# Optimization experiments

Measured on AMD Instinct MI355X. Metric: run time of the kernel, lower is better.

The kernel has to match this reference:

```python
import jax, jax.numpy as jnp
import numpy as np

B, S, D, H = 4, 4096, 1024, 64

def setup_inputs() -> dict:
    key = jax.random.key(0)
    k1, k2, k3, k4 = jax.random.split(key, 4)
    inp = {
        'input': jax.random.normal(k1, (B, S, D), dtype=jnp.float32),
        'Wq': jax.random.normal(k2, (D, H), dtype=jnp.float32) * (D ** -0.5),
        'Wk': jax.random.normal(k3, (D, H), dtype=jnp.float32) * (D ** -0.5),
        'Wv': jax.random.normal(k4, (D, H), dtype=jnp.float32) * (D ** -0.5),
    }
    return inp

def reference(input, Wq, Wk, Wv):
    # Projections: [B,S,D] @ [D,H] -> [B,S,H]
    q = input @ Wq
    k = input @ Wk
    v = input @ Wv
    head_size = Wq.shape[-1]
    # Scaled scores: [B,S,S]
    scores = jnp.einsum('bqh,bkh->bqk', q, k) * (head_size ** -0.5)
    seq_len = input.shape[1]
    causal = jnp.tril(jnp.ones((seq_len, seq_len), dtype=bool))
    masked = jnp.where(causal, scores, -jnp.inf)
    weights = jax.nn.softmax(masked, axis=-1)
    # dropout p=0.0 -> identity
    return jnp.einsum('bqk,bkh->bqh', weights, v)
```

## Files before the change

### kernel.cpp

```cpp
#include <hip/hip_runtime.h>

#define NS 8

typedef __attribute__((ext_vector_type(8))) short sh8;
typedef __attribute__((ext_vector_type(4))) short sh4;
typedef __attribute__((ext_vector_type(4))) float f4;

#define QSCALE 0.18033688011112042f

typedef const __attribute__((address_space(1))) unsigned int* gas_t;
typedef __attribute__((address_space(3))) unsigned int* las_t;
#define GLD16(g, l) __builtin_amdgcn_global_load_lds((gas_t)(g), (las_t)(l), 16, 0, 0)

static __device__ __forceinline__ unsigned short f2bf(float f) {
  unsigned u = __builtin_bit_cast(unsigned, f);
  u += 0x7fffu + ((u >> 16) & 1u);
  return (unsigned short)(u >> 16);
}
static __device__ __forceinline__ float bf2f(unsigned short s) {
  unsigned u = ((unsigned)s) << 16;
  return __builtin_bit_cast(float, u);
}

__global__ __launch_bounds__(256) void wt_kernel(const float* __restrict__ Wq,
                                                 const float* __restrict__ Wk,
                                                 const float* __restrict__ Wv,
                                                 unsigned short* __restrict__ Wt2) {
  int blk = blockIdx.x;
  int band = blk >> 3;
  int widx = band >> 2;
  const float* W = widx == 0 ? Wq : (widx == 1 ? Wk : Wv);
  int ncol = (band & 3) * 16;
  int t = threadIdx.x;
  int kt = (blk & 7) * 4 + (t >> 6);
  int lane = t & 63, q = lane >> 4, l15 = lane & 15;
  const float* src = W + (size_t)(kt * 32 + q * 8) * 64 + ncol + l15;
  sh8 o;
#pragma unroll
  for (int j = 0; j < 8; ++j) o[j] = (short)f2bf(src[(size_t)j * 64]);
  *(sh8*)&Wt2[((size_t)(band * 32 + kt) * 64 + lane) * 8] = o;
}

__global__ __launch_bounds__(256, 1) void proj_kernel(const float* __restrict__ in,
                                                      const unsigned short* __restrict__ Wt2,
                                                      unsigned short* __restrict__ Qg,
                                                      unsigned short* __restrict__ Kg,
                                                      unsigned short* __restrict__ Vtg) {
  __shared__ __align__(16) char lds[131072];
  int t = threadIdx.x;
  int w = t >> 6, lane = t & 63, q = lane >> 4, l15 = lane & 15;
  int m0 = blockIdx.x * 32;

  const float* ga = in + (size_t)(m0 + (w >> 1) * 16 + l15) * 1024 + q * 8 + (w & 1) * 4;
  const unsigned short* gb = Wt2 + (size_t)(w * 3) * 16384 + lane * 8;

  f4 acc[2][3];
  f4 z = {0.f, 0.f, 0.f, 0.f};
#pragma unroll
  for (int mt = 0; mt < 2; ++mt)
#pragma unroll
    for (int nt = 0; nt < 3; ++nt) acc[mt][nt] = z;

#define STAGE(s, buf)                                                         \
  {                                                                           \
    char* base = lds + (buf) * 65536;                                         \
    const float* gas = ga + (s) * 128;                                        \
    _Pragma("unroll")                                                         \
    for (int kk = 0; kk < 4; ++kk) {                                          \
      GLD16(gas + kk * 32, base + kk * 4096 + w * 1024);                      \
      _Pragma("unroll")                                                       \
      for (int nt = 0; nt < 3; ++nt)                                          \
        GLD16(gb + nt * 16384 + ((s) * 4 + kk) * 512,                         \
              base + 16384 + (kk * 12 + w * 3 + nt) * 1024);                  \
    }                                                                         \
  }

  STAGE(0, 0);
  for (int s = 0; s < 8; ++s) {
    int cur = s & 1;
    __syncthreads();
    if (s + 1 < 8) STAGE(s + 1, cur ^ 1);

    const f4* Af = (const f4*)(lds + cur * 65536);
    const sh8* Bf = (const sh8*)(lds + cur * 65536 + 16384);
#pragma unroll
    for (int kk = 0; kk < 4; ++kk) {
      sh8 bfr[3];
#pragma unroll
      for (int nt = 0; nt < 3; ++nt)
        bfr[nt] = Bf[(kk * 12 + w * 3 + nt) * 64 + lane];
#pragma unroll
      for (int mt = 0; mt < 2; ++mt) {
        f4 lo = Af[kk * 256 + mt * 128 + lane];
        f4 hi = Af[kk * 256 + mt * 128 + 64 + lane];
        sh8 a;
#pragma unroll
        for (int j = 0; j < 4; ++j) {
          a[j] = (short)f2bf(lo[j]);
          a[4 + j] = (short)f2bf(hi[j]);
        }
#pragma unroll
        for (int nt = 0; nt < 3; ++nt)
          acc[mt][nt] = __builtin_amdgcn_mfma_f32_16x16x32_bf16(a, bfr[nt], acc[mt][nt], 0, 0, 0);
      }
    }
  }
#undef STAGE

  float* vred = (float*)lds;
#pragma unroll
  for (int nt = 0; nt < 3; ++nt) {
    int band = w * 3 + nt;
#pragma unroll
    for (int mt = 0; mt < 2; ++mt)
#pragma unroll
      for (int r = 0; r < 4; ++r) {
        int row = mt * 16 + q * 4 + r;
        float v = acc[mt][nt][r];
        if (band < 4) {
          Qg[(size_t)(m0 + row) * 64 + band * 16 + l15] = f2bf(v * QSCALE);
        } else if (band < 8) {
          Kg[(size_t)(m0 + row) * 64 + (band - 4) * 16 + l15] = f2bf(v);
        } else {
          vred[row * 69 + (band - 8) * 16 + l15] = v;
        }
      }
  }
  __syncthreads();
  {
    int h = t >> 2, sl = (t & 3) * 8;
    int bb = m0 >> 12, s0 = m0 & 4095;
    sh8 vv;
#pragma unroll
    for (int j = 0; j < 8; ++j) vv[j] = (short)f2bf(vred[(sl + j) * 69 + h]);
    *(sh8*)&Vtg[(((size_t)(bb * 64 + h)) << 12) + s0 + sl] = vv;
  }
}

__global__ __launch_bounds__(256, 4) void attn_split(const unsigned short* __restrict__ Qg,
                                                     const unsigned short* __restrict__ Kg,
                                                     const unsigned short* __restrict__ Vtg,
                                                     unsigned short* __restrict__ Opart,
                                                     float* __restrict__ Lpart) {
  __shared__ unsigned short Ks[64 * 72];
  __shared__ unsigned short Vs[64 * 72];
  __shared__ unsigned short Pw[4 * 16 * 72];
  int t = threadIdx.x;
  int b = blockIdx.y;
  int qt = 63 - (int)(blockIdx.x >> 3);
  int sp = blockIdx.x & 7;
  int wave = t >> 6, lane = t & 63, quad = lane >> 4, l15 = lane & 15;
  unsigned short* Pws = Pw + wave * 16 * 72;

  int qrow0 = qt * 64 + wave * 16;
  size_t pbase = ((size_t)sp * 4 + b) * 4096;

  int nkt = qt + 1;
  int chunk = (nkt + NS - 1) / NS;
  int t0 = sp * chunk, t1 = min(nkt, t0 + chunk);
  if (t0 >= t1) {
#pragma unroll
    for (int r = 0; r < 4; ++r) {
      size_t row = pbase + qrow0 + quad * 4 + r;
#pragma unroll
      for (int ht = 0; ht < 4; ++ht) Opart[row * 64 + ht * 16 + l15] = 0;
      if (l15 == 0) Lpart[row] = 0.f;
    }
    return;
  }

  sh8 qa[2];
#pragma unroll
  for (int ks = 0; ks < 2; ++ks)
    qa[ks] = *(const sh8*)&Qg[(size_t)((b << 12) + qrow0 + l15) * 64 + ks * 32 + quad * 8];

  sh8 ones;
#pragma unroll
  for (int j = 0; j < 8; ++j) ones[j] = (short)0x3F80;

  f4 o[5];
  f4 z = {0.f, 0.f, 0.f, 0.f};
#pragma unroll
  for (int ht = 0; ht < 5; ++ht) o[ht] = z;

  int r0 = t >> 3, o0 = (t & 7) * 8;
  int r1 = (t + 256) >> 3, o1 = ((t + 256) & 7) * 8;
  const unsigned short* kg0 = Kg + (size_t)((b << 12) + r0) * 64 + o0;
  const unsigned short* kg1 = Kg + (size_t)((b << 12) + r1) * 64 + o1;
  const unsigned short* vg0 = Vtg + (((size_t)(b * 64 + r0)) << 12) + o0;
  const unsigned short* vg1 = Vtg + (((size_t)(b * 64 + r1)) << 12) + o1;

  sh8 kr0, kr1, vr0, vr1;
  {
    size_t ko = (size_t)t0 * 64 * 64;
    kr0 = *(const sh8*)(kg0 + ko); kr1 = *(const sh8*)(kg1 + ko);
    vr0 = *(const sh8*)(vg0 + t0 * 64); vr1 = *(const sh8*)(vg1 + t0 * 64);
  }

  for (int kt = t0; kt < t1; ++kt) {
    __syncthreads();
    *(sh8*)&Ks[r0 * 72 + o0] = kr0;
    *(sh8*)&Ks[r1 * 72 + o1] = kr1;
    *(sh8*)&Vs[r0 * 72 + o0] = vr0;
    *(sh8*)&Vs[r1 * 72 + o1] = vr1;
    if (kt + 1 < t1) {
      size_t ko = (size_t)(kt + 1) * 64 * 64;
      kr0 = *(const sh8*)(kg0 + ko); kr1 = *(const sh8*)(kg1 + ko);
      vr0 = *(const sh8*)(vg0 + (kt + 1) * 64); vr1 = *(const sh8*)(vg1 + (kt + 1) * 64);
    }
    __syncthreads();

    f4 st[4];
#pragma unroll
    for (int nt = 0; nt < 4; ++nt) st[nt] = z;
#pragma unroll
    for (int ks = 0; ks < 2; ++ks) {
#pragma unroll
      for (int nt = 0; nt < 4; ++nt) {
        sh8 kb = *(const sh8*)&Ks[(nt * 16 + l15) * 72 + ks * 32 + quad * 8];
        st[nt] = __builtin_amdgcn_mfma_f32_16x16x32_bf16(kb, qa[ks], st[nt], 0, 0, 0);
      }
    }

    if (kt == nkt - 1) {
      int qrow = qrow0 + l15;
#pragma unroll
      for (int nt = 0; nt < 4; ++nt) {
        int key0 = kt * 64 + nt * 16 + quad * 4;
#pragma unroll
        for (int r = 0; r < 4; ++r)
          if (key0 + r > qrow) st[nt][r] = -__builtin_inff();
      }
    }

#pragma unroll
    for (int nt = 0; nt < 4; ++nt) {
      sh4 pk;
#pragma unroll
      for (int r = 0; r < 4; ++r) pk[r] = (short)f2bf(exp2f(st[nt][r]));
      *(sh4*)&Pws[l15 * 72 + nt * 16 + quad * 4] = pk;
    }
    asm volatile("s_waitcnt lgkmcnt(0)" ::: "memory");

#pragma unroll
    for (int ks = 0; ks < 2; ++ks) {
      sh8 pa = *(const sh8*)&Pws[l15 * 72 + ks * 32 + quad * 8];
#pragma unroll
      for (int ht = 0; ht < 4; ++ht) {
        sh8 vb = *(const sh8*)&Vs[(ht * 16 + l15) * 72 + ks * 32 + quad * 8];
        o[ht] = __builtin_amdgcn_mfma_f32_16x16x32_bf16(pa, vb, o[ht], 0, 0, 0);
      }
      o[4] = __builtin_amdgcn_mfma_f32_16x16x32_bf16(pa, ones, o[4], 0, 0, 0);
    }
  }

#pragma unroll
  for (int r = 0; r < 4; ++r) {
    size_t row = pbase + qrow0 + quad * 4 + r;
#pragma unroll
    for (int ht = 0; ht < 4; ++ht)
      Opart[row * 64 + ht * 16 + l15] = f2bf(o[ht][r]);
    if (l15 == 0) Lpart[row] = o[4][r];
  }
}

__global__ __launch_bounds__(256) void attn_combine(const unsigned short* __restrict__ Opart,
                                                    const float* __restrict__ Lpart,
                                                    float* __restrict__ out) {
  int t = threadIdx.x;
  int r = blockIdx.x * 32 + (t >> 3);
  int h0 = (t & 7) * 8;
  float L = 0.f;
  float acc[8];
#pragma unroll
  for (int j = 0; j < 8; ++j) acc[j] = 0.f;
#pragma unroll
  for (int s = 0; s < NS; ++s) {
    L += Lpart[(size_t)s * 16384 + r];
    sh8 v = *(const sh8*)&Opart[((size_t)s * 16384 + r) * 64 + h0];
#pragma unroll
    for (int j = 0; j < 8; ++j) acc[j] += bf2f((unsigned short)v[j]);
  }
  float inv = 1.f / L;
  f4 o0, o1;
#pragma unroll
  for (int j = 0; j < 4; ++j) { o0[j] = acc[j] * inv; o1[j] = acc[4 + j] * inv; }
  *(f4*)&out[(size_t)r * 64 + h0] = o0;
  *(f4*)&out[(size_t)r * 64 + h0 + 4] = o1;
}

extern "C" void kernel_launch(void* const* d_in, const int* in_sizes, int n_in,
                              void* d_out, int out_size, void* d_ws, size_t ws_size,
                              hipStream_t stream) {
  const float* in = (const float*)d_in[0];
  const float* Wq = (const float*)d_in[1];
  const float* Wk = (const float*)d_in[2];
  const float* Wv = (const float*)d_in[3];
  float* out = (float*)d_out;

  char* ws = (char*)d_ws;
  unsigned short* Wt2   = (unsigned short*)ws;
  unsigned short* Qg    = (unsigned short*)(ws + 393216);
  unsigned short* Kg    = (unsigned short*)(ws + 2490368);
  unsigned short* Vtg   = (unsigned short*)(ws + 4587520);
  unsigned short* Opart = (unsigned short*)(ws + 6684672);
  float*          Lpart = (float*)(ws + 23461888);

  hipLaunchKernelGGL(wt_kernel, dim3(96), dim3(256), 0, stream, Wq, Wk, Wv, Wt2);
  hipLaunchKernelGGL(proj_kernel, dim3(512), dim3(256), 0, stream, in, Wt2, Qg, Kg, Vtg);
  hipLaunchKernelGGL(attn_split, dim3(64 * NS, 4), dim3(256), 0, stream,
                     Qg, Kg, Vtg, Opart, Lpart);
  hipLaunchKernelGGL(attn_combine, dim3(512), dim3(256), 0, stream,
                     Opart, Lpart, out);
}
```

Measured before the change: 150.1 us.

## Widen attention key tile to 128 keys per iteration with larger LDS buffers

Each loop iteration of the split attention kernel now processes 128 keys instead of 64: K and transposed V tiles in LDS are doubled and each thread prefetches four vectors of K and V per step. The P@V phase runs in two 64-key halves reusing the same per-wave P scratch. This halves the number of barrier-separated iterations and loads per key block, at the cost of more LDS and registers (launch bound lowered from 4 to 3 blocks per CU). It also does more masked wasted work on the diagonal tile and makes split chunks coarser, which may hurt load balance.

```diff
diff --git a/kernel.cpp b/kernel.cpp
--- a/kernel.cpp
+++ b/kernel.cpp
@@ -137,13 +137,13 @@
   }
 }
 
-__global__ __launch_bounds__(256, 4) void attn_split(const unsigned short* __restrict__ Qg,
+__global__ __launch_bounds__(256, 3) void attn_split(const unsigned short* __restrict__ Qg,
                                                      const unsigned short* __restrict__ Kg,
                                                      const unsigned short* __restrict__ Vtg,
                                                      unsigned short* __restrict__ Opart,
                                                      float* __restrict__ Lpart) {
-  __shared__ unsigned short Ks[64 * 72];
-  __shared__ unsigned short Vs[64 * 72];
+  __shared__ unsigned short Ks[128 * 72];
+  __shared__ unsigned short Vs[64 * 136];
   __shared__ unsigned short Pw[4 * 16 * 72];
   int t = threadIdx.x;
   int b = blockIdx.y;
@@ -155,9 +155,9 @@
   int qrow0 = qt * 64 + wave * 16;
   size_t pbase = ((size_t)sp * 4 + b) * 4096;
 
-  int nkt = qt + 1;
-  int chunk = (nkt + NS - 1) / NS;
-  int t0 = sp * chunk, t1 = min(nkt, t0 + chunk);
+  int KT = (qt + 2) >> 1;
+  int chunk = (KT + NS - 1) / NS;
+  int t0 = sp * chunk, t1 = min(KT, t0 + chunk);
   if (t0 >= t1) {
 #pragma unroll
     for (int r = 0; r < 4; ++r) {
@@ -183,50 +183,55 @@
 #pragma unroll
   for (int ht = 0; ht < 5; ++ht) o[ht] = z;
 
-  int r0 = t >> 3, o0 = (t & 7) * 8;
-  int r1 = (t + 256) >> 3, o1 = ((t + 256) & 7) * 8;
-  const unsigned short* kg0 = Kg + (size_t)((b << 12) + r0) * 64 + o0;
-  const unsigned short* kg1 = Kg + (size_t)((b << 12) + r1) * 64 + o1;
-  const unsigned short* vg0 = Vtg + (((size_t)(b * 64 + r0)) << 12) + o0;
-  const unsigned short* vg1 = Vtg + (((size_t)(b * 64 + r1)) << 12) + o1;
-
-  sh8 kr0, kr1, vr0, vr1;
+  int r0 = t >> 3, koff = (t & 7) * 8;
+  int v0 = t >> 4, voff = (t & 15) * 8;
+  const unsigned short* kg = Kg + ((size_t)(b << 12) + r0) * 64 + koff;
+  const unsigned short* vg = Vtg + (((size_t)(b * 64 + v0)) << 12) + voff;
+
+  sh8 kpr[4], vpr[4];
   {
-    size_t ko = (size_t)t0 * 64 * 64;
-    kr0 = *(const sh8*)(kg0 + ko); kr1 = *(const sh8*)(kg1 + ko);
-    vr0 = *(const sh8*)(vg0 + t0 * 64); vr1 = *(const sh8*)(vg1 + t0 * 64);
+    size_t ko = (size_t)t0 * 8192;
+#pragma unroll
+    for (int s = 0; s < 4; ++s) {
+      kpr[s] = *(const sh8*)(kg + ko + s * 2048);
+      vpr[s] = *(const sh8*)(vg + (size_t)t0 * 128 + (size_t)s * 65536);
+    }
   }
 
   for (int kt = t0; kt < t1; ++kt) {
     __syncthreads();
-    *(sh8*)&Ks[r0 * 72 + o0] = kr0;
-    *(sh8*)&Ks[r1 * 72 + o1] = kr1;
-    *(sh8*)&Vs[r0 * 72 + o0] = vr0;
-    *(sh8*)&Vs[r1 * 72 + o1] = vr1;
+#pragma unroll
+    for (int s = 0; s < 4; ++s) {
+      *(sh8*)&Ks[(r0 + 32 * s) * 72 + koff] = kpr[s];
+      *(sh8*)&Vs[(v0 + 16 * s) * 136 + voff] = vpr[s];
+    }
     if (kt + 1 < t1) {
-      size_t ko = (size_t)(kt + 1) * 64 * 64;
-      kr0 = *(const sh8*)(kg0 + ko); kr1 = *(const sh8*)(kg1 + ko);
-      vr0 = *(const sh8*)(vg0 + (kt + 1) * 64); vr1 = *(const sh8*)(vg1 + (kt + 1) * 64);
+      size_t ko = (size_t)(kt + 1) * 8192;
+#pragma unroll
+      for (int s = 0; s < 4; ++s) {
+        kpr[s] = *(const sh8*)(kg + ko + s * 2048);
+        vpr[s] = *(const sh8*)(vg + (size_t)(kt + 1) * 128 + (size_t)s * 65536);
+      }
     }
     __syncthreads();
 
-    f4 st[4];
-#pragma unroll
-    for (int nt = 0; nt < 4; ++nt) st[nt] = z;
+    f4 st[8];
+#pragma unroll
+    for (int nt = 0; nt < 8; ++nt) st[nt] = z;
 #pragma unroll
     for (int ks = 0; ks < 2; ++ks) {
 #pragma unroll
-      for (int nt = 0; nt < 4; ++nt) {
+      for (int nt = 0; nt < 8; ++nt) {
         sh8 kb = *(const sh8*)&Ks[(nt * 16 + l15) * 72 + ks * 32 + quad * 8];
         st[nt] = __builtin_amdgcn_mfma_f32_16x16x32_bf16(kb, qa[ks], st[nt], 0, 0, 0);
       }
     }
 
-    if (kt == nkt - 1) {
+    if (kt == KT - 1) {
       int qrow = qrow0 + l15;
 #pragma unroll
-      for (int nt = 0; nt < 4; ++nt) {
-        int key0 = kt * 64 + nt * 16 + quad * 4;
+      for (int nt = 0; nt < 8; ++nt) {
+        int key0 = kt * 128 + nt * 16 + quad * 4;
 #pragma unroll
         for (int r = 0; r < 4; ++r)
           if (key0 + r > qrow) st[nt][r] = -__builtin_inff();
@@ -234,23 +239,26 @@
     }
 
 #pragma unroll
-    for (int nt = 0; nt < 4; ++nt) {
-      sh4 pk;
-#pragma unroll
-      for (int r = 0; r < 4; ++r) pk[r] = (short)f2bf(exp2f(st[nt][r]));
-      *(sh4*)&Pws[l15 * 72 + nt * 16 + quad * 4] = pk;
-    }
-    asm volatile("s_waitcnt lgkmcnt(0)" ::: "memory");
-
-#pragma unroll
-    for (int ks = 0; ks < 2; ++ks) {
-      sh8 pa = *(const sh8*)&Pws[l15 * 72 + ks * 32 + quad * 8];
-#pragma unroll
-      for (int ht = 0; ht < 4; ++ht) {
-        sh8 vb = *(const sh8*)&Vs[(ht * 16 + l15) * 72 + ks * 32 + quad * 8];
-        o[ht] = __builtin_amdgcn_mfma_f32_16x16x32_bf16(pa, vb, o[ht], 0, 0, 0);
-      }
-      o[4] = __builtin_amdgcn_mfma_f32_16x16x32_bf16(pa, ones, o[4], 0, 0, 0);
+    for (int half = 0; half < 2; ++half) {
+#pragma unroll
+      for (int nt = 0; nt < 4; ++nt) {
+        sh4 pk;
+#pragma unroll
+        for (int r = 0; r < 4; ++r) pk[r] = (short)f2bf(exp2f(st[half * 4 + nt][r]));
+        *(sh4*)&Pws[l15 * 72 + nt * 16 + quad * 4] = pk;
+      }
+      asm volatile("s_waitcnt lgkmcnt(0)" ::: "memory");
+
+#pragma unroll
+      for (int ks = 0; ks < 2; ++ks) {
+        sh8 pa = *(const sh8*)&Pws[l15 * 72 + ks * 32 + quad * 8];
+#pragma unroll
+        for (int ht = 0; ht < 4; ++ht) {
+          sh8 vb = *(const sh8*)&Vs[(ht * 16 + l15) * 136 + half * 64 + ks * 32 + quad * 8];
+          o[ht] = __builtin_amdgcn_mfma_f32_16x16x32_bf16(pa, vb, o[ht], 0, 0, 0);
+        }
+        o[4] = __builtin_amdgcn_mfma_f32_16x16x32_bf16(pa, ones, o[4], 0, 0, 0);
+      }
     }
   }
 
```

New measurement: 154.6 us. +3.0%, slower.
